# Kernel optimization log

Measured on AMD Instinct MI355X. Metric: run time of the kernel, lower is better.

Reference implementation:

```python
import jax, jax.numpy as jnp
import numpy as np

B, S, D_IN, H, G, HD = 1, 2048, 2048, 32, 8, 128
GS = H // G  # group_size = 4
D_OUT = H * HD  # 4096
EPS = 1e-6


def _rmsnorm(x, scale):
    # qwen3-compatible: compute in fp32 over last dim
    xf = x.astype(jnp.float32)
    var = jnp.mean(xf * xf, axis=-1, keepdims=True)
    return (xf * jax.lax.rsqrt(var + EPS) * scale).astype(x.dtype)


def _apply_rope(x, cos, sin):
    # x: [b, h, s, d]; cos/sin: [s, d]
    d2 = x.shape[-1] // 2
    x1, x2 = x[..., :d2], x[..., d2:]
    rotated = jnp.concatenate([-x2, x1], axis=-1)
    return (x * cos[None, None] + rotated * sin[None, None]).astype(x.dtype)


def setup_inputs() -> dict:
    key = jax.random.key(0)
    ks = jax.random.split(key, 8)
    x = jax.random.normal(ks[0], (B, S, D_IN), jnp.float32)
    mask = jnp.triu(jnp.ones((S, S), bool), k=1)  # causal: True = masked
    # RoPE tables [S, HD]
    inv_freq = 1.0 / (10000.0 ** (jnp.arange(0, HD, 2, dtype=jnp.float32) / HD))
    ang = jnp.arange(S, dtype=jnp.float32)[:, None] * inv_freq[None, :]
    ang = jnp.concatenate([ang, ang], axis=-1)
    cos, sin = jnp.cos(ang), jnp.sin(ang)
    std = 0.02
    Wq = jax.random.normal(ks[1], (D_IN, D_OUT), jnp.float32) * std
    Wk = jax.random.normal(ks[2], (D_IN, G * HD), jnp.float32) * std
    Wv = jax.random.normal(ks[3], (D_IN, G * HD), jnp.float32) * std
    Wo = jax.random.normal(ks[4], (D_OUT, D_IN), jnp.float32) * std
    q_scale = jnp.ones((HD,), jnp.float32)
    k_scale = jnp.ones((HD,), jnp.float32)
    return {"x": x, "mask": mask, "cos": cos, "sin": sin,
            "Wq": Wq, "Wk": Wk, "Wv": Wv, "Wo": Wo,
            "q_scale": q_scale, "k_scale": k_scale}


def reference(x, mask, cos, sin, Wq, Wk, Wv, Wo, q_scale, k_scale):
    b, s, _ = x.shape
    q = (x @ Wq).reshape(b, s, H, HD).transpose(0, 2, 1, 3)   # [b,H,s,hd]
    k = (x @ Wk).reshape(b, s, G, HD).transpose(0, 2, 1, 3)   # [b,G,s,hd]
    v = (x @ Wv).reshape(b, s, G, HD).transpose(0, 2, 1, 3)   # [b,G,s,hd]
    q = _rmsnorm(q, q_scale)
    k = _rmsnorm(k, k_scale)
    q = _apply_rope(q, cos[:s], sin[:s])
    k = _apply_rope(k, cos[:s], sin[:s])
    next_k, next_v = k, v  # cache (num_kv_groups heads)
    # GQA via broadcasting instead of repeat_interleave (same math)
    qg = q.reshape(b, G, GS, s, HD)
    scores = jnp.einsum('bgrsd,bgtd->bgrst', qg, k)           # [b,G,gs,s,s]
    scores = jnp.where(mask[None, None, None], -jnp.inf, scores)
    attn = jax.nn.softmax(scores / np.sqrt(HD).astype(np.float32), axis=-1)
    ctx = jnp.einsum('bgrst,bgtd->bgrsd', attn, v)            # [b,G,gs,s,hd]
    ctx = ctx.reshape(b, H, s, HD).transpose(0, 2, 1, 3).reshape(b, s, D_OUT)
    out = ctx @ Wo
    return out, next_k, next_v
```

## Files before the change

### kernel.cpp

```cpp
#include <hip/hip_runtime.h>

typedef unsigned short ushort_t;
typedef short short8 __attribute__((ext_vector_type(8)));
typedef float floatx4 __attribute__((ext_vector_type(4)));

#define S_LEN 2048
#define DIN   2048
#define NH    32
#define NG    8
#define HDIM  128
#define DOUT  4096
#define DKV   1024
#define QLD   6144

__device__ __forceinline__ float b2f(ushort_t u) {
  union { float f; unsigned u; } t; t.u = ((unsigned)u) << 16; return t.f;
}
__device__ __forceinline__ ushort_t f2b(float f) {
  union { float f; unsigned u; } t; t.f = f;
  unsigned v = t.u;
  v += 0x7FFFu + ((v >> 16) & 1u);
  return (ushort_t)(v >> 16);
}

__device__ __forceinline__ void glds16(const ushort_t* g, ushort_t* l) {
  __builtin_amdgcn_global_load_lds((const __attribute__((address_space(1))) void*)g,
                                   (__attribute__((address_space(3))) void*)l, 16, 0, 0);
}

__global__ __launch_bounds__(256) void tcast(const float* __restrict__ W,
                                             ushort_t* __restrict__ Wt,
                                             int N, int ldt) {
  __shared__ float t[32][33];
  const int bx = blockIdx.x * 32;
  const int by = blockIdx.y * 32;
  const int tx = threadIdx.x & 31;
  const int ty = threadIdx.x >> 5;
#pragma unroll
  for (int i = 0; i < 32; i += 8)
    t[ty + i][tx] = W[(size_t)(by + ty + i) * N + bx + tx];
  __syncthreads();
#pragma unroll
  for (int i = 0; i < 32; i += 8)
    Wt[(size_t)(bx + ty + i) * ldt + by + tx] = f2b(t[tx][ty + i]);
}

__global__ __launch_bounds__(256) void castx(const float* __restrict__ x,
                                             ushort_t* __restrict__ xb) {
  const size_t i = ((size_t)blockIdx.x * 256 + threadIdx.x) * 4;
  float4 v = *(const float4*)&x[i];
  union { int2 p; ushort_t s[4]; } w;
  w.s[0] = f2b(v.x); w.s[1] = f2b(v.y); w.s[2] = f2b(v.z); w.s[3] = f2b(v.w);
  *(int2*)&xb[i] = w.p;
}

template <int CF32, int BM>
__global__ __launch_bounds__(256) void gemm_glds(const ushort_t* __restrict__ A, int lda,
                                                 const ushort_t* __restrict__ Bt, int ldb,
                                                 void* __restrict__ Cp, int ldc, int K) {
  constexpr int MI = BM / 32;
  __shared__ __align__(16) ushort_t As[2][BM * 32];
  __shared__ __align__(16) ushort_t Bs[2][4096];
  const int tid  = threadIdx.x;
  const int m0   = blockIdx.y * BM;
  const int n0   = blockIdx.x * 128;
  const int wave = tid >> 6, lane = tid & 63;
  const int lrow = lane & 15, quad = lane >> 4;
  const int wm = (wave >> 1) * (BM / 2), wn = (wave & 1) * 64;

  floatx4 acc[MI][4];
#pragma unroll
  for (int mi = 0; mi < MI; mi++)
#pragma unroll
    for (int ni = 0; ni < 4; ni++)
#pragma unroll
      for (int j = 0; j < 4; j++) acc[mi][ni][j] = 0.0f;

  const int sc = ((tid & 3) ^ ((tid >> 3) & 3)) * 8;
  const ushort_t* ag0 = A + (size_t)(m0 + (tid >> 2)) * lda + sc;
  const ushort_t* ag1 = ag0 + (size_t)64 * lda;
  const ushort_t* bg0 = Bt + (size_t)(n0 + (tid >> 2)) * ldb + sc;
  const ushort_t* bg1 = bg0 + (size_t)64 * ldb;
  const int so = wave * 512;

  auto stage = [&](int k0, int b) {
    glds16(ag0 + k0, &As[b][so]);
    if constexpr (BM == 128) glds16(ag1 + k0, &As[b][2048 + so]);
    glds16(bg0 + k0, &Bs[b][so]);
    glds16(bg1 + k0, &Bs[b][2048 + so]);
  };

  const int rq = (quad ^ ((lrow >> 1) & 3)) * 8;

  auto compute = [&](int b) {
    short8 af[MI], bfr[4];
#pragma unroll
    for (int mi = 0; mi < MI; mi++)
      af[mi] = *(const short8*)&As[b][(wm + mi * 16 + lrow) * 32 + rq];
#pragma unroll
    for (int ni = 0; ni < 4; ni++)
      bfr[ni] = *(const short8*)&Bs[b][(wn + ni * 16 + lrow) * 32 + rq];
#pragma unroll
    for (int mi = 0; mi < MI; mi++)
#pragma unroll
      for (int ni = 0; ni < 4; ni++)
        acc[mi][ni] = __builtin_amdgcn_mfma_f32_16x16x32_bf16(af[mi], bfr[ni], acc[mi][ni], 0, 0, 0);
  };

  stage(0, 0);
  asm volatile("s_waitcnt vmcnt(0)" ::: "memory");
  __builtin_amdgcn_s_barrier();

  const int NT = K >> 5;
  for (int t = 0; t < NT; t += 2) {
    stage((t + 1) << 5, 1);
    compute(0);
    asm volatile("s_waitcnt vmcnt(0)" ::: "memory");
    __builtin_amdgcn_s_barrier();
    if (t + 2 < NT) stage((t + 2) << 5, 0);
    compute(1);
    asm volatile("s_waitcnt vmcnt(0)" ::: "memory");
    __builtin_amdgcn_s_barrier();
  }

#pragma unroll
  for (int mi = 0; mi < MI; mi++)
#pragma unroll
    for (int ni = 0; ni < 4; ni++)
#pragma unroll
      for (int i = 0; i < 4; i++) {
        const int row = m0 + wm + mi * 16 + quad * 4 + i;
        const int col = n0 + wn + ni * 16 + lrow;
        if (CF32) ((float*)Cp)[(size_t)row * ldc + col] = acc[mi][ni][i];
        else      ((ushort_t*)Cp)[(size_t)row * ldc + col] = f2b(acc[mi][ni][i]);
      }
}

__global__ __launch_bounds__(256) void norm_qk(ushort_t* __restrict__ qkv,
                                               const float* __restrict__ cosb,
                                               const float* __restrict__ sinb,
                                               const float* __restrict__ qs,
                                               const float* __restrict__ ks,
                                               ushort_t* __restrict__ kb) {
  const int idx  = blockIdx.x * 4 + (threadIdx.x >> 6);
  const int lane = threadIdx.x & 63;
  const int SH = S_LEN * NH;
  const float QSC = 0.08838834764831845f * 1.4426950408889634f;

  if (idx < SH) {
    const int s = idx >> 5, h = idx & 31;
    ushort_t* row = qkv + (size_t)s * QLD + h * HDIM;
    float x1 = b2f(row[lane]), x2 = b2f(row[lane + 64]);
    float ss = x1 * x1 + x2 * x2;
#pragma unroll
    for (int off = 1; off < 64; off <<= 1) ss += __shfl_xor(ss, off);
    const float inv = rsqrtf(ss * (1.0f / 128.0f) + 1e-6f);
    const float y1 = x1 * inv * qs[lane] * QSC;
    const float y2 = x2 * inv * qs[lane + 64] * QSC;
    const float c1 = cosb[s * HDIM + lane],      s1 = sinb[s * HDIM + lane];
    const float c2 = cosb[s * HDIM + lane + 64], s2 = sinb[s * HDIM + lane + 64];
    row[lane]      = f2b(y1 * c1 - y2 * s1);
    row[lane + 64] = f2b(y2 * c2 + y1 * s2);
  } else {
    const int j = idx - SH;
    const int s = j >> 3, g = j & 7;
    const ushort_t* row = qkv + (size_t)s * QLD + DOUT + g * HDIM;
    float x1 = b2f(row[lane]), x2 = b2f(row[lane + 64]);
    float ss = x1 * x1 + x2 * x2;
#pragma unroll
    for (int off = 1; off < 64; off <<= 1) ss += __shfl_xor(ss, off);
    const float inv = rsqrtf(ss * (1.0f / 128.0f) + 1e-6f);
    const float y1 = x1 * inv * ks[lane];
    const float y2 = x2 * inv * ks[lane + 64];
    const float c1 = cosb[s * HDIM + lane],      s1 = sinb[s * HDIM + lane];
    const float c2 = cosb[s * HDIM + lane + 64], s2 = sinb[s * HDIM + lane + 64];
    ushort_t* o = kb + ((size_t)g * S_LEN + s) * HDIM;
    o[lane]      = f2b(y1 * c1 - y2 * s1);
    o[lane + 64] = f2b(y2 * c2 + y1 * s2);
  }
}

__global__ __launch_bounds__(256) void vtrans(const ushort_t* __restrict__ qkv,
                                              ushort_t* __restrict__ vt) {
  __shared__ ushort_t t[64][65];
  const int g = blockIdx.x;
  const int s0 = blockIdx.y * 64, d0 = blockIdx.z * 64;
  const int tx = threadIdx.x & 63, ty = threadIdx.x >> 6;
#pragma unroll
  for (int i = 0; i < 64; i += 4)
    t[ty + i][tx] = qkv[(size_t)(s0 + ty + i) * QLD + DOUT + DKV + g * HDIM + d0 + tx];
  __syncthreads();
#pragma unroll
  for (int i = 0; i < 64; i += 4)
    vt[((size_t)(g * HDIM + d0 + ty + i)) * S_LEN + s0 + tx] = t[tx][ty + i];
}

__global__ __launch_bounds__(256, 2) void attn(ushort_t* QC,
                                               const ushort_t* __restrict__ Kb,
                                               const ushort_t* __restrict__ Vt) {
  __shared__ __align__(16) ushort_t Ks[2][8192];
  __shared__ __align__(16) ushort_t Vs[2][8192];
  __shared__ __align__(16) ushort_t Ps[64 * 72];
  const int h  = blockIdx.x;
  const int qt = 31 - blockIdx.y;
  const int g  = h >> 2;
  const int tid = threadIdx.x;
  const int wave = tid >> 6, lane = tid & 63;
  const int lrow = lane & 15, quad = lane >> 4;
  const ushort_t* Kg = Kb + (size_t)g * S_LEN * HDIM;
  const ushort_t* Vg = Vt + (size_t)g * HDIM * S_LEN;
  const int r0 = qt * 64;
  const int qrow0 = r0 + wave * 16;

  short8 qf[4];
#pragma unroll
  for (int kd = 0; kd < 4; kd++)
    qf[kd] = *(const short8*)&QC[(size_t)(qrow0 + lrow) * QLD + h * HDIM + kd * 32 + quad * 8];

  short8 vones;
#pragma unroll
  for (int j = 0; j < 8; j++) vones[j] = (lrow == 0) ? (short)0x3F80 : (short)0;

  floatx4 ctx[8], ctxl;
#pragma unroll
  for (int nd = 0; nd < 8; nd++)
#pragma unroll
    for (int j = 0; j < 4; j++) ctx[nd][j] = 0.0f;
#pragma unroll
  for (int j = 0; j < 4; j++) ctxl[j] = 0.0f;

  const int swz = ((lane & 3) ^ ((lane >> 3) & 3)) * 8;
  const ushort_t* kgl = Kg + (size_t)(wave * 16 + (lane >> 2)) * HDIM + swz;
  const ushort_t* vgl = Vg + (size_t)(wave * 32 + (lane >> 2)) * S_LEN + swz;

  auto stageKV = [&](int t0, int b) {
#pragma unroll
    for (int i = 0; i < 4; i++)
      glds16(kgl + (size_t)t0 * HDIM + i * 32, &Ks[b][i * 2048 + wave * 512]);
#pragma unroll
    for (int i = 0; i < 4; i++)
      glds16(vgl + (size_t)((i >> 1) * 16) * S_LEN + t0 + (i & 1) * 32,
             &Vs[b][(i & 1) * 4096 + (wave * 32 + (i >> 1) * 16) * 32]);
  };

  const int rq = (quad ^ ((lrow >> 1) & 3)) * 8;

  stageKV(0, 0);
  asm volatile("s_waitcnt vmcnt(0)" ::: "memory");
  __builtin_amdgcn_s_barrier();

  int buf = 0;
  for (int t0 = 0; t0 <= r0; t0 += 64) {
    if (t0 + 64 <= r0) stageKV(t0 + 64, buf ^ 1);
    const ushort_t* Kc = Ks[buf];
    const ushort_t* Vc = Vs[buf];

    floatx4 sacc[4];
#pragma unroll
    for (int ni = 0; ni < 4; ni++)
#pragma unroll
      for (int j = 0; j < 4; j++) sacc[ni][j] = 0.0f;
#pragma unroll
    for (int kd = 0; kd < 4; kd++) {
      short8 kf[4];
#pragma unroll
      for (int ni = 0; ni < 4; ni++)
        kf[ni] = *(const short8*)&Kc[kd * 2048 + (ni * 16 + lrow) * 32 + rq];
#pragma unroll
      for (int ni = 0; ni < 4; ni++)
        sacc[ni] = __builtin_amdgcn_mfma_f32_16x16x32_bf16(qf[kd], kf[ni], sacc[ni], 0, 0, 0);
    }

    const bool diag = (t0 == r0);
#pragma unroll
    for (int ni = 0; ni < 4; ni++)
#pragma unroll
      for (int i = 0; i < 4; i++) {
        float sv = sacc[ni][i];
        if (diag && (t0 + ni * 16 + lrow > qrow0 + quad * 4 + i)) sv = -1e30f;
        sacc[ni][i] = exp2f(sv - 17.0f);
      }

#pragma unroll
    for (int ni = 0; ni < 4; ni++)
#pragma unroll
      for (int i = 0; i < 4; i++)
        Ps[(wave * 16 + quad * 4 + i) * 72 + ni * 16 + lrow] = f2b(sacc[ni][i]);
    asm volatile("s_waitcnt lgkmcnt(0)" ::: "memory");

#pragma unroll
    for (int kt = 0; kt < 2; kt++) {
      const short8 pf = *(const short8*)&Ps[(wave * 16 + lrow) * 72 + kt * 32 + quad * 8];
      ctxl = __builtin_amdgcn_mfma_f32_16x16x32_bf16(pf, vones, ctxl, 0, 0, 0);
#pragma unroll
      for (int nd = 0; nd < 8; nd++) {
        const short8 vf = *(const short8*)&Vc[kt * 4096 + (nd * 16 + lrow) * 32 + rq];
        ctx[nd] = __builtin_amdgcn_mfma_f32_16x16x32_bf16(pf, vf, ctx[nd], 0, 0, 0);
      }
    }

    asm volatile("s_waitcnt vmcnt(0)" ::: "memory");
    __builtin_amdgcn_s_barrier();
    buf ^= 1;
  }

  float invl[4];
#pragma unroll
  for (int i = 0; i < 4; i++) invl[i] = 1.0f / __shfl(ctxl[i], lane & 48);

  __syncthreads();
  ushort_t* Es = (wave < 2) ? Ks[0] : Vs[0];
  const int eb = (wave & 1) * 16;
#pragma unroll
  for (int i = 0; i < 4; i++)
#pragma unroll
    for (int nd = 0; nd < 8; nd++)
      Es[(eb + quad * 4 + i) * 136 + nd * 16 + lrow] = f2b(ctx[nd][i] * invl[i]);
  asm volatile("s_waitcnt lgkmcnt(0)" ::: "memory");
  const int erow = lane >> 4;
  const int ecol = (lane & 15) * 8;
#pragma unroll
  for (int rr = 0; rr < 4; rr++) {
    int4 v = *(const int4*)&Es[(eb + rr * 4 + erow) * 136 + ecol];
    *(int4*)&QC[(size_t)(r0 + wave * 16 + rr * 4 + erow) * QLD + h * HDIM + ecol] = v;
  }
}

__global__ __launch_bounds__(256) void fink(const ushort_t* __restrict__ kb,
                                            float* __restrict__ nk) {
  const size_t e = ((size_t)blockIdx.x * 256 + threadIdx.x) * 8;
  union { int4 v; ushort_t s[8]; } u;
  u.v = *(const int4*)&kb[e];
#pragma unroll
  for (int j = 0; j < 8; j++) nk[e + j] = b2f(u.s[j]);
}

__global__ __launch_bounds__(256) void finv(const ushort_t* __restrict__ qkv,
                                            float* __restrict__ nv) {
  const int s = blockIdx.x;
  const int g = threadIdx.x >> 5, d4 = (threadIdx.x & 31) * 4;
  union { short4 v; ushort_t s[4]; } u;
  u.v = *(const short4*)&qkv[(size_t)s * QLD + DOUT + DKV + g * HDIM + d4];
  float4 o;
  o.x = b2f(u.s[0]); o.y = b2f(u.s[1]); o.z = b2f(u.s[2]); o.w = b2f(u.s[3]);
  *(float4*)&nv[((size_t)g * S_LEN + s) * HDIM + d4] = o;
}

extern "C" void kernel_launch(void* const* d_in, const int* in_sizes, int n_in,
                              void* d_out, int out_size, void* d_ws, size_t ws_size,
                              hipStream_t stream) {
  const float* x    = (const float*)d_in[0];
  const float* cosb = (const float*)d_in[2];
  const float* sinb = (const float*)d_in[3];
  const float* Wq   = (const float*)d_in[4];
  const float* Wk   = (const float*)d_in[5];
  const float* Wv   = (const float*)d_in[6];
  const float* Wo   = (const float*)d_in[7];
  const float* qs   = (const float*)d_in[8];
  const float* ks   = (const float*)d_in[9];

  float* outf = (float*)d_out;
  float* nkf  = outf + (size_t)S_LEN * DIN;
  float* nvf  = nkf + (size_t)NG * S_LEN * HDIM;

  const size_t MiB = 1024 * 1024;
  ushort_t* WallT = (ushort_t*)d_out;
  ushort_t* xb    = (ushort_t*)((char*)d_out + 24 * MiB);
  ushort_t* WoT   = (ushort_t*)((char*)d_out + 16 * MiB);
  ushort_t* vt    = (ushort_t*)d_out;
  ushort_t* qkv   = (ushort_t*)d_ws;
  ushort_t* kb    = (ushort_t*)((char*)d_ws + 24 * MiB);

  tcast<<<dim3(128, 64), 256, 0, stream>>>(Wq, WallT, DOUT, DIN);
  tcast<<<dim3(32, 64), 256, 0, stream>>>(Wk, WallT + (size_t)4096 * DIN, DKV, DIN);
  tcast<<<dim3(32, 64), 256, 0, stream>>>(Wv, WallT + (size_t)5120 * DIN, DKV, DIN);
  castx<<<4096, 256, 0, stream>>>(x, xb);

  gemm_glds<0, 128><<<dim3(48, 16), 256, 0, stream>>>(xb, DIN, WallT, DIN, qkv, QLD, DIN);

  tcast<<<dim3(64, 128), 256, 0, stream>>>(Wo, WoT, DIN, DOUT);

  norm_qk<<<(S_LEN * NH + S_LEN * NG) / 4, 256, 0, stream>>>(qkv, cosb, sinb, qs, ks, kb);

  vtrans<<<dim3(NG, S_LEN / 64, HDIM / 64), 256, 0, stream>>>(qkv, vt);

  attn<<<dim3(NH, 32), 256, 0, stream>>>(qkv, kb, vt);

  gemm_glds<1, 64><<<dim3(16, 32), 256, 0, stream>>>(qkv, QLD, WoT, DOUT, outf, DIN, DOUT);

  fink<<<1024, 256, 0, stream>>>(kb, nkf);
  finv<<<S_LEN, 256, 0, stream>>>(qkv, nvf);
}
```

Before: 410.6 us.

## Triple-buffer GEMM loads and deepen attention KV prefetch with partial vmcnt waits

The GEMM moves from a double-buffered loop that drains all loads every step to a three-stage ring buffer. Partial vmcnt waits keep two tiles of global-to-LDS loads in flight while the current tile is computed. The attention kernel likewise prefetches two KV tiles ahead with partial waits, issuing the next stage only after a barrier once the current buffer has been consumed. MFMA sections are wrapped in s_setprio to favor the matrix issue; the cost is more LDS per GEMM block, which may reduce occupancy, and waitcnt values that are fragile if the load count changes.

```diff
diff --git a/kernel.cpp b/kernel.cpp
--- a/kernel.cpp
+++ b/kernel.cpp
@@ -59,8 +59,8 @@
                                                  const ushort_t* __restrict__ Bt, int ldb,
                                                  void* __restrict__ Cp, int ldc, int K) {
   constexpr int MI = BM / 32;
-  __shared__ __align__(16) ushort_t As[2][BM * 32];
-  __shared__ __align__(16) ushort_t Bs[2][4096];
+  __shared__ __align__(16) ushort_t As[3][BM * 32];
+  __shared__ __align__(16) ushort_t Bs[3][4096];
   const int tid  = threadIdx.x;
   const int m0   = blockIdx.y * BM;
   const int n0   = blockIdx.x * 128;
@@ -83,45 +83,59 @@
   const ushort_t* bg1 = bg0 + (size_t)64 * ldb;
   const int so = wave * 512;
 
-  auto stage = [&](int k0, int b) {
-    glds16(ag0 + k0, &As[b][so]);
-    if constexpr (BM == 128) glds16(ag1 + k0, &As[b][2048 + so]);
-    glds16(bg0 + k0, &Bs[b][so]);
-    glds16(bg1 + k0, &Bs[b][2048 + so]);
+  auto stage = [&](int k0, ushort_t* aB, ushort_t* bB) {
+    glds16(ag0 + k0, aB + so);
+    if constexpr (BM == 128) glds16(ag1 + k0, aB + 2048 + so);
+    glds16(bg0 + k0, bB + so);
+    glds16(bg1 + k0, bB + 2048 + so);
   };
 
   const int rq = (quad ^ ((lrow >> 1) & 3)) * 8;
 
-  auto compute = [&](int b) {
+  stage(0,  As[0], Bs[0]);
+  stage(32, As[1], Bs[1]);
+  stage(64, As[2], Bs[2]);
+
+  ushort_t *a_cur = As[0], *a_n1 = As[1], *a_n2 = As[2];
+  ushort_t *b_cur = Bs[0], *b_n1 = Bs[1], *b_n2 = Bs[2];
+
+  const int NT = K >> 5;
+  for (int t = 0; t < NT; t++) {
+    if (t + 2 < NT) {
+      if constexpr (BM == 128) asm volatile("s_waitcnt vmcnt(8)" ::: "memory");
+      else                     asm volatile("s_waitcnt vmcnt(6)" ::: "memory");
+    } else if (t + 1 < NT) {
+      if constexpr (BM == 128) asm volatile("s_waitcnt vmcnt(4)" ::: "memory");
+      else                     asm volatile("s_waitcnt vmcnt(3)" ::: "memory");
+    } else {
+      asm volatile("s_waitcnt vmcnt(0)" ::: "memory");
+    }
+    __builtin_amdgcn_s_barrier();
+
     short8 af[MI], bfr[4];
 #pragma unroll
     for (int mi = 0; mi < MI; mi++)
-      af[mi] = *(const short8*)&As[b][(wm + mi * 16 + lrow) * 32 + rq];
-#pragma unroll
-    for (int ni = 0; ni < 4; ni++)
-      bfr[ni] = *(const short8*)&Bs[b][(wn + ni * 16 + lrow) * 32 + rq];
+      af[mi] = *(const short8*)&a_cur[(wm + mi * 16 + lrow) * 32 + rq];
+#pragma unroll
+    for (int ni = 0; ni < 4; ni++)
+      bfr[ni] = *(const short8*)&b_cur[(wn + ni * 16 + lrow) * 32 + rq];
+    asm volatile("s_waitcnt lgkmcnt(0)" ::: "memory");
+    __builtin_amdgcn_s_barrier();
+
+    if (t + 3 < NT) stage((t + 3) << 5, a_cur, b_cur);
+
+    __builtin_amdgcn_s_setprio(1);
 #pragma unroll
     for (int mi = 0; mi < MI; mi++)
 #pragma unroll
       for (int ni = 0; ni < 4; ni++)
         acc[mi][ni] = __builtin_amdgcn_mfma_f32_16x16x32_bf16(af[mi], bfr[ni], acc[mi][ni], 0, 0, 0);
-  };
-
-  stage(0, 0);
+    __builtin_amdgcn_s_setprio(0);
+
+    ushort_t* ta = a_cur; a_cur = a_n1; a_n1 = a_n2; a_n2 = ta;
+    ushort_t* tb = b_cur; b_cur = b_n1; b_n1 = b_n2; b_n2 = tb;
+  }
   asm volatile("s_waitcnt vmcnt(0)" ::: "memory");
-  __builtin_amdgcn_s_barrier();
-
-  const int NT = K >> 5;
-  for (int t = 0; t < NT; t += 2) {
-    stage((t + 1) << 5, 1);
-    compute(0);
-    asm volatile("s_waitcnt vmcnt(0)" ::: "memory");
-    __builtin_amdgcn_s_barrier();
-    if (t + 2 < NT) stage((t + 2) << 5, 0);
-    compute(1);
-    asm volatile("s_waitcnt vmcnt(0)" ::: "memory");
-    __builtin_amdgcn_s_barrier();
-  }
 
 #pragma unroll
   for (int mi = 0; mi < MI; mi++)
@@ -246,12 +260,13 @@
   const int rq = (quad ^ ((lrow >> 1) & 3)) * 8;
 
   stageKV(0, 0);
-  asm volatile("s_waitcnt vmcnt(0)" ::: "memory");
-  __builtin_amdgcn_s_barrier();
+  if (r0 > 0) stageKV(64, 1);
 
   int buf = 0;
   for (int t0 = 0; t0 <= r0; t0 += 64) {
-    if (t0 + 64 <= r0) stageKV(t0 + 64, buf ^ 1);
+    if (t0 < r0) asm volatile("s_waitcnt vmcnt(8)" ::: "memory");
+    else         asm volatile("s_waitcnt vmcnt(0)" ::: "memory");
+    __builtin_amdgcn_s_barrier();
     const ushort_t* Kc = Ks[buf];
     const ushort_t* Vc = Vs[buf];
 
@@ -260,6 +275,7 @@
     for (int ni = 0; ni < 4; ni++)
 #pragma unroll
       for (int j = 0; j < 4; j++) sacc[ni][j] = 0.0f;
+    __builtin_amdgcn_s_setprio(1);
 #pragma unroll
     for (int kd = 0; kd < 4; kd++) {
       short8 kf[4];
@@ -270,6 +286,7 @@
       for (int ni = 0; ni < 4; ni++)
         sacc[ni] = __builtin_amdgcn_mfma_f32_16x16x32_bf16(qf[kd], kf[ni], sacc[ni], 0, 0, 0);
     }
+    __builtin_amdgcn_s_setprio(0);
 
     const bool diag = (t0 == r0);
 #pragma unroll
@@ -288,6 +305,7 @@
         Ps[(wave * 16 + quad * 4 + i) * 72 + ni * 16 + lrow] = f2b(sacc[ni][i]);
     asm volatile("s_waitcnt lgkmcnt(0)" ::: "memory");
 
+    __builtin_amdgcn_s_setprio(1);
 #pragma unroll
     for (int kt = 0; kt < 2; kt++) {
       const short8 pf = *(const short8*)&Ps[(wave * 16 + lrow) * 72 + kt * 32 + quad * 8];
@@ -298,9 +316,11 @@
         ctx[nd] = __builtin_amdgcn_mfma_f32_16x16x32_bf16(pf, vf, ctx[nd], 0, 0, 0);
       }
     }
-
-    asm volatile("s_waitcnt vmcnt(0)" ::: "memory");
+    __builtin_amdgcn_s_setprio(0);
+
+    asm volatile("s_waitcnt lgkmcnt(0)" ::: "memory");
     __builtin_amdgcn_s_barrier();
+    if (t0 + 128 <= r0) stageKV(t0 + 128, buf);
     buf ^= 1;
   }
 
@@ -308,6 +328,7 @@
 #pragma unroll
   for (int i = 0; i < 4; i++) invl[i] = 1.0f / __shfl(ctxl[i], lane & 48);
 
+  asm volatile("s_waitcnt vmcnt(0)" ::: "memory");
   __syncthreads();
   ushort_t* Es = (wave < 2) ? Ks[0] : Vs[0];
   const int eb = (wave & 1) * 16;
```

Result: faster. 376.9 us (-8.2%).
